# Kernel tuning notes

Hardware: AMD Instinct MI355X
Metric: run time of the kernel (lower is better)

The kernel has to match this reference:

```python
import jax, jax.numpy as jnp
import numpy as np

V, F, P = 1024, 2048, 8192
_EPS = 1e-12


def setup_inputs() -> dict:
    key = jax.random.key(0)
    kv, kf, kp = jax.random.split(key, 3)
    verts = jax.random.normal(kv, (V, 3), dtype=jnp.float32)
    faces = jax.random.randint(kf, (F, 3), 0, V, dtype=jnp.int32)
    points = jax.random.normal(kp, (P, 3), dtype=jnp.float32)
    return {"verts": verts, "faces": faces, "points": points}


def _closest_point_on_tri(p, a, b, c):
    """Ericson's closest-point-on-triangle, broadcast over leading dims.
    p, a, b, c: [..., 3] -> closest point [..., 3]."""
    ab = b - a
    ac = c - a
    ap = p - a
    d1 = jnp.sum(ab * ap, -1)
    d2 = jnp.sum(ac * ap, -1)
    bp = p - b
    d3 = jnp.sum(ab * bp, -1)
    d4 = jnp.sum(ac * bp, -1)
    cp = p - c
    d5 = jnp.sum(ab * cp, -1)
    d6 = jnp.sum(ac * cp, -1)
    vc = d1 * d4 - d3 * d2
    vb = d5 * d2 - d1 * d6
    va = d3 * d6 - d5 * d4
    # guarded edge/interior parameters (denominators are >0 whenever the
    # corresponding region condition holds; eps keeps unselected branches finite)
    t_ab = d1 / jnp.maximum(d1 - d3, _EPS)
    t_ac = d2 / jnp.maximum(d2 - d6, _EPS)
    t_bc = (d4 - d3) / jnp.maximum((d4 - d3) + (d5 - d6), _EPS)
    denom = jnp.maximum(va + vb + vc, _EPS)
    v_in = vb / denom
    w_in = vc / denom
    # first-match region selection (vertex A, vertex B, edge AB, vertex C, edge AC, edge BC, interior)
    cA = (d1 <= 0) & (d2 <= 0)
    cB = (d3 >= 0) & (d4 <= d3)
    cAB = (vc <= 0) & (d1 >= 0) & (d3 <= 0)
    cC = (d6 >= 0) & (d5 <= d6)
    cAC = (vb <= 0) & (d2 >= 0) & (d6 <= 0)
    cBC = (va <= 0) & ((d4 - d3) >= 0) & ((d5 - d6) >= 0)
    z = jnp.zeros_like(d1)
    o = jnp.ones_like(d1)
    bv = jnp.select([cA, cB, cAB, cC, cAC, cBC], [z, o, t_ab, z, z, 1.0 - t_bc], v_in)
    bw = jnp.select([cA, cB, cAB, cC, cAC, cBC], [z, z, z, o, t_ac, t_bc], w_in)
    bu = 1.0 - bv - bw
    return a * bu[..., None] + b * bv[..., None] + c * bw[..., None]


def reference(verts, faces, points):
    tri = verts[faces]  # [F, 3, 3]
    a = tri[:, 0][None]  # [1, F, 3]
    b = tri[:, 1][None]
    c = tri[:, 2][None]
    cp = _closest_point_on_tri(points[:, None, :], a, b, c)  # [P, F, 3]
    dist2 = jnp.sum((points[:, None, :] - cp) ** 2, -1)  # [P, F] squared distances
    assoc = jnp.argmin(dist2, axis=1).astype(jnp.int32)  # [P] nearest triangle index
    dist = jnp.min(dist2, axis=1)  # [P]
    # loss_type == 'mse': kernel loss = sum(dist), then *= 1000 / P
    loss = jnp.sum(dist) * (1000.0 / points.shape[0])
    return loss, dist, assoc
```

## Files before the change

kernel.cpp:

```cpp
#include <hip/hip_runtime.h>
#include <float.h>

#define P_TOTAL 8192
#define F_TOTAL 2048
#define TPB     256
#define CHUNK   256
#define HALF_T  (F_TOTAL / 2)
#define NCHUNK  (HALF_T / CHUNK)

__device__ __forceinline__ float refine_rcp(float D) {
#pragma clang fp contract(off)
    float r0 = __builtin_amdgcn_rcpf(D);
    float e1 = __builtin_fmaf(-D, r0, 1.0f);
    return __builtin_fmaf(e1, r0, r0);
}
__device__ __forceinline__ float div_rn(float num, float D, float r) {
#pragma clang fp contract(off)
    float q0 = num * r;
    float e  = __builtin_fmaf(-D, q0, num);
    return __builtin_fmaf(e, r, q0);
}

__device__ __forceinline__ void region_select(
    float d1, float d2, float d3, float d4, float d5, float d6,
    float va, float vb, float vc, float d43, float d56,
    float g1, float g2, float g3, float g4,
    float& bu, float& bv, float& bw)
{
#pragma clang fp contract(off)
    float G1 = fmaxf(g1, 1e-12f);
    float G2 = fmaxf(g2, 1e-12f);
    float G3 = fmaxf(g3, 1e-12f);
    float G4 = fmaxf(g4, 1e-12f);

    bool cA  = (d1 <= 0.f) & (d2 <= 0.f);
    bool cB  = (d3 >= 0.f) & (d4 <= d3);
    bool cAB = (vc <= 0.f) & (d1 >= 0.f) & (d3 <= 0.f);
    bool cC  = (d6 >= 0.f) & (d5 <= d6);
    bool cAC = (vb <= 0.f) & (d2 >= 0.f) & (d6 <= 0.f);
    bool cBC = (va <= 0.f) & (d43 >= 0.f) & (d56 >= 0.f);

    float nv = cA ? 0.f : cB ? 1.f : cAB ? d1 : cC ? 0.f
             : cAC ? 0.f : cBC ? d43 : vb;
    float nw = cA ? 0.f : cB ? 0.f : cAB ? 0.f : cC ? 1.f
             : cAC ? d2 : cBC ? d43 : vc;
    float D  = cA ? 1.f : cB ? 1.f : cAB ? G1 : cC ? 1.f
             : cAC ? G2 : cBC ? G3 : G4;
    bool fBC = cBC && !(cA || cB || cAB || cC || cAC);

    float r   = refine_rcp(D);
    float qv  = div_rn(nv, D, r);
    float bww = div_rn(nw, D, r);
    float bvv = fBC ? (1.0f - qv) : qv;
    bv = bvv; bw = bww;
    bu = (1.0f - bvv) - bww;
}

__device__ __forceinline__ float eval_exact(
    float px, float py, float pz, float4 q0, float4 q1, float4 q2)
{
#pragma clang fp contract(off)
    float ax = q0.x, ay = q0.y, az = q0.z;
    float bx = q0.w, by = q1.x, bz = q1.y;
    float cx = q1.z, cy = q1.w, cz = q2.x;

    float abx = bx - ax, aby = by - ay, abz = bz - az;
    float acx = cx - ax, acy = cy - ay, acz = cz - az;
    float apx = px - ax, apy = py - ay, apz = pz - az;
    float d1 = (abx * apx + aby * apy) + abz * apz;
    float d2 = (acx * apx + acy * apy) + acz * apz;
    float bpx = px - bx, bpy = py - by, bpz = pz - bz;
    float d3 = (abx * bpx + aby * bpy) + abz * bpz;
    float d4 = (acx * bpx + acy * bpy) + acz * bpz;
    float cpx = px - cx, cpy = py - cy, cpz = pz - cz;
    float d5 = (abx * cpx + aby * cpy) + abz * cpz;
    float d6 = (acx * cpx + acy * cpy) + acz * cpz;

    float vc = d1 * d4 - d3 * d2;
    float vb = d5 * d2 - d1 * d6;
    float va = d3 * d6 - d5 * d4;
    float d43 = d4 - d3, d56 = d5 - d6;
    float g1 = d1 - d3, g2 = d2 - d6, g3 = d43 + d56, g4 = (va + vb) + vc;

    float bu, bv, bw;
    region_select(d1, d2, d3, d4, d5, d6, va, vb, vc, d43, d56,
                  g1, g2, g3, g4, bu, bv, bw);

    float cpx2 = (ax * bu + bx * bv) + cx * bw;
    float cpy2 = (ay * bu + by * bv) + cy * bw;
    float cpz2 = (az * bu + bz * bv) + cz * bw;
    float dx = px - cpx2, dy = py - cpy2, dz = pz - cpz2;
    return (dx * dx + dy * dy) + dz * dz;
}

__global__ __launch_bounds__(256) void msdf_prep(
    const float* __restrict__ verts, const int* __restrict__ faces,
    float4* __restrict__ pre_n, float4* __restrict__ pre_v,
    float4* __restrict__ pre_a)
{
    int t = blockIdx.x * 256 + threadIdx.x;
    int i0 = faces[3 * t + 0], i1 = faces[3 * t + 1], i2 = faces[3 * t + 2];
    float ax = verts[3 * i0], ay = verts[3 * i0 + 1], az = verts[3 * i0 + 2];
    float bx = verts[3 * i1], by = verts[3 * i1 + 1], bz = verts[3 * i1 + 2];
    float cx = verts[3 * i2], cy = verts[3 * i2 + 1], cz = verts[3 * i2 + 2];
    float e1x = bx - ax, e1y = by - ay, e1z = bz - az;
    float e2x = cx - ax, e2y = cy - ay, e2z = cz - az;
    float nx = e1y * e2z - e1z * e2y;
    float ny = e1z * e2x - e1x * e2z;
    float nz = e1x * e2y - e1y * e2x;
    float nn = (nx * nx + ny * ny) + nz * nz;
    float inv = (nn > 1e-30f) ? (1.0f / sqrtf(nn)) : 0.0f;
    nx *= inv; ny *= inv; nz *= inv;
    pre_n[t] = make_float4(nx, ny, nz, (nx * ax + ny * ay) + nz * az);
    pre_v[3 * t + 0] = make_float4(ax, ay, az, bx);
    pre_v[3 * t + 1] = make_float4(by, bz, cx, cy);
    pre_v[3 * t + 2] = make_float4(cz, 0.f, 0.f, 0.f);
    pre_a[t] = make_float4(ax, ay, az, 0.f);
}

#define FLUSH_BODY(take) do {                                             \
    int j = (lane < (take)) ? lane : 0;                                   \
    int t = slist[w][(h + j) & 511];                                      \
    float4 q0 = pre_v[3 * t + 0];                                         \
    float4 q1 = pre_v[3 * t + 1];                                         \
    float4 q2 = pre_v[3 * t + 2];                                         \
    float d2v = eval_exact(px, py, pz, q0, q1, q2);                       \
    unsigned int bits = __float_as_uint(d2v);                             \
    if (bits < best_bits) { best_bits = bits; best_idx = t; }             \
    ubloc = fminf(ubloc, d2v);                                            \
    h += (take); pend -= (take);                                          \
} while (0)

__global__ __launch_bounds__(TPB) void msdf_main(
    const float4* __restrict__ pre_n, const float4* __restrict__ pre_v,
    const float4* __restrict__ pre_a,
    const float* __restrict__ points, float* __restrict__ out)
{
    __shared__ int slist[4][512];
    __shared__ unsigned long long keys[4];
    const int tid  = threadIdx.x;
    const int lane = tid & 63;
    const int w    = tid >> 6;
    const int p    = blockIdx.x * 2 + (w >> 1);
    const int tb   = (w & 1) * HALF_T;

    const float px = points[3 * p], py = points[3 * p + 1], pz = points[3 * p + 2];

    float u = FLT_MAX;
    #pragma unroll
    for (int s = 0; s < 4; ++s) {
        float4 q = pre_a[tb + s * 64 + lane];
        float dx = px - q.x, dy = py - q.y, dz = pz - q.z;
        u = fminf(u, (dx * dx + dy * dy) + dz * dz);
    }
    #pragma unroll
    for (int off = 32; off; off >>= 1)
        u = fminf(u, __shfl_xor(u, off, 64));
    float ub = u;

    unsigned int best_bits = 0xFFFFFFFFu;
    int best_idx = 0;
    int pend = 0, h = 0;

    for (int c = 0; c < NCHUNK; ++c) {
        const float ubm = ub * 1.02f + 1e-18f;
        #pragma unroll
        for (int s = 0; s < 4; ++s) {
            int t = tb + c * CHUNK + s * 64 + lane;
            float4 n = pre_n[t];
            float lv = ((n.x * px + n.y * py) + n.z * pz) - n.w;
            bool pred = (lv * lv <= ubm);
            unsigned long long m = __ballot(pred);
            if (pred) {
                int off = (int)__popcll(m & ((1ull << lane) - 1ull));
                slist[w][(h + pend + off) & 511] = t;
            }
            pend += (int)__popcll(m);
        }

        bool drain = (c == 0) || (c == NCHUNK - 1);
        if (pend >= 64 || (drain && pend > 0)) {
            float ubloc = FLT_MAX;
            while (pend >= 64) FLUSH_BODY(64);
            if (drain && pend > 0) FLUSH_BODY(pend);
            #pragma unroll
            for (int off = 32; off; off >>= 1)
                ubloc = fminf(ubloc, __shfl_xor(ubloc, off, 64));
            ub = fminf(ub, ubloc);
        }
    }

    unsigned long long key =
        ((unsigned long long)best_bits << 32) | (unsigned int)best_idx;
    #pragma unroll
    for (int off = 32; off > 0; off >>= 1) {
        unsigned int hi = (unsigned int)(key >> 32);
        unsigned int lo = (unsigned int)(key & 0xFFFFFFFFu);
        unsigned int ohi = __shfl_down(hi, off, 64);
        unsigned int olo = __shfl_down(lo, off, 64);
        unsigned long long ok = ((unsigned long long)ohi << 32) | olo;
        key = (ok < key) ? ok : key;
    }
    if (lane == 0) keys[w] = key;
    __syncthreads();
    if (tid < 2) {
        unsigned long long k0 = keys[2 * tid];
        unsigned long long k1 = keys[2 * tid + 1];
        unsigned long long km = (k1 < k0) ? k1 : k0;
        int pp = blockIdx.x * 2 + tid;
        out[1 + pp]           = __uint_as_float((unsigned int)(km >> 32));
        out[1 + P_TOTAL + pp] = (float)(unsigned int)(km & 0xFFFFFFFFu);
    }
}

__global__ __launch_bounds__(256) void msdf_loss(float* __restrict__ out)
{
    __shared__ float wsum[4];
    float s = 0.f;
    for (int k = 0; k < P_TOTAL / 256; ++k)
        s += out[1 + k * 256 + threadIdx.x];
    #pragma unroll
    for (int off = 32; off > 0; off >>= 1) s += __shfl_down(s, off, 64);
    int lane = threadIdx.x & 63, w = threadIdx.x >> 6;
    if (lane == 0) wsum[w] = s;
    __syncthreads();
    if (threadIdx.x == 0) {
        float tot = ((wsum[0] + wsum[1]) + wsum[2]) + wsum[3];
        out[0] = tot * (1000.0f / (float)P_TOTAL);
    }
}

extern "C" void kernel_launch(void* const* d_in, const int* in_sizes, int n_in,
                              void* d_out, int out_size, void* d_ws, size_t ws_size,
                              hipStream_t stream) {
    const float* verts  = (const float*)d_in[0];
    const int*   faces  = (const int*)d_in[1];
    const float* points = (const float*)d_in[2];
    float* out = (float*)d_out;
    float4* pre_n = (float4*)d_ws;
    float4* pre_v = (float4*)((char*)d_ws + F_TOTAL * 16);
    float4* pre_a = (float4*)((char*)d_ws + F_TOTAL * 16 * 4);

    msdf_prep<<<dim3(F_TOTAL / 256), dim3(256), 0, stream>>>(verts, faces, pre_n, pre_v, pre_a);
    msdf_main<<<dim3(P_TOTAL / 2), dim3(TPB), 0, stream>>>(pre_n, pre_v, pre_a, points, out);
    msdf_loss<<<dim3(1), dim3(256), 0, stream>>>(out);
}
```

Before: 87.18 us.

## Split each point across four waves and fuse loss via last-block reduction

```diff
diff --git a/kernel.cpp b/kernel.cpp
--- a/kernel.cpp
+++ b/kernel.cpp
@@ -5,8 +5,10 @@
 #define F_TOTAL 2048
 #define TPB     256
 #define CHUNK   256
-#define HALF_T  (F_TOTAL / 2)
-#define NCHUNK  (HALF_T / CHUNK)
+#define QUART_T (F_TOTAL / 4)
+#define NCHUNK  (QUART_T / CHUNK)
+
+__device__ unsigned int g_cnt;
 
 __device__ __forceinline__ float refine_rcp(float D) {
 #pragma clang fp contract(off)
@@ -98,6 +100,7 @@
     float4* __restrict__ pre_n, float4* __restrict__ pre_v,
     float4* __restrict__ pre_a)
 {
+    if (blockIdx.x == 0 && threadIdx.x == 0) g_cnt = 0u;
     int t = blockIdx.x * 256 + threadIdx.x;
     int i0 = faces[3 * t + 0], i1 = faces[3 * t + 1], i2 = faces[3 * t + 2];
     float ax = verts[3 * i0], ay = verts[3 * i0 + 1], az = verts[3 * i0 + 2];
@@ -138,11 +141,14 @@
 {
     __shared__ int slist[4][512];
     __shared__ unsigned long long keys[4];
+    __shared__ float ubsh[4];
+    __shared__ float wsum[4];
+    __shared__ int amLast;
     const int tid  = threadIdx.x;
     const int lane = tid & 63;
     const int w    = tid >> 6;
-    const int p    = blockIdx.x * 2 + (w >> 1);
-    const int tb   = (w & 1) * HALF_T;
+    const int p    = blockIdx.x;
+    const int tb   = w * QUART_T;
 
     const float px = points[3 * p], py = points[3 * p + 1], pz = points[3 * p + 2];
 
@@ -156,7 +162,9 @@
     #pragma unroll
     for (int off = 32; off; off >>= 1)
         u = fminf(u, __shfl_xor(u, off, 64));
-    float ub = u;
+    if (lane == 0) ubsh[w] = u;
+    __syncthreads();
+    float ub = fminf(fminf(ubsh[0], ubsh[1]), fminf(ubsh[2], ubsh[3]));
 
     unsigned int best_bits = 0xFFFFFFFFu;
     int best_idx = 0;
@@ -178,15 +186,18 @@
             pend += (int)__popcll(m);
         }
 
-        bool drain = (c == 0) || (c == NCHUNK - 1);
-        if (pend >= 64 || (drain && pend > 0)) {
-            float ubloc = FLT_MAX;
-            while (pend >= 64) FLUSH_BODY(64);
-            if (drain && pend > 0) FLUSH_BODY(pend);
-            #pragma unroll
-            for (int off = 32; off; off >>= 1)
-                ubloc = fminf(ubloc, __shfl_xor(ubloc, off, 64));
-            ub = fminf(ub, ubloc);
+        float ubloc = FLT_MAX;
+        while (pend >= 64) FLUSH_BODY(64);
+        if (pend > 0) FLUSH_BODY(pend);
+        #pragma unroll
+        for (int off = 32; off; off >>= 1)
+            ubloc = fminf(ubloc, __shfl_xor(ubloc, off, 64));
+        ub = fminf(ub, ubloc);
+
+        if (c == 0) {
+            if (lane == 0) ubsh[w] = ub;
+            __syncthreads();
+            ub = fminf(fminf(ubsh[0], ubsh[1]), fminf(ubsh[2], ubsh[3]));
         }
     }
 
@@ -203,30 +214,32 @@
     }
     if (lane == 0) keys[w] = key;
     __syncthreads();
-    if (tid < 2) {
-        unsigned long long k0 = keys[2 * tid];
-        unsigned long long k1 = keys[2 * tid + 1];
-        unsigned long long km = (k1 < k0) ? k1 : k0;
-        int pp = blockIdx.x * 2 + tid;
-        out[1 + pp]           = __uint_as_float((unsigned int)(km >> 32));
-        out[1 + P_TOTAL + pp] = (float)(unsigned int)(km & 0xFFFFFFFFu);
-    }
-}
-
-__global__ __launch_bounds__(256) void msdf_loss(float* __restrict__ out)
-{
-    __shared__ float wsum[4];
-    float s = 0.f;
-    for (int k = 0; k < P_TOTAL / 256; ++k)
-        s += out[1 + k * 256 + threadIdx.x];
-    #pragma unroll
-    for (int off = 32; off > 0; off >>= 1) s += __shfl_down(s, off, 64);
-    int lane = threadIdx.x & 63, w = threadIdx.x >> 6;
-    if (lane == 0) wsum[w] = s;
+    if (tid == 0) {
+        unsigned long long k0 = keys[0], k1 = keys[1];
+        unsigned long long k2 = keys[2], k3 = keys[3];
+        unsigned long long ka = (k1 < k0) ? k1 : k0;
+        unsigned long long kb = (k3 < k2) ? k3 : k2;
+        unsigned long long km = (kb < ka) ? kb : ka;
+        out[1 + p]           = __uint_as_float((unsigned int)(km >> 32));
+        out[1 + P_TOTAL + p] = (float)(unsigned int)(km & 0xFFFFFFFFu);
+        __threadfence();
+        amLast = (atomicAdd(&g_cnt, 1u) == (unsigned int)(gridDim.x - 1));
+    }
     __syncthreads();
-    if (threadIdx.x == 0) {
-        float tot = ((wsum[0] + wsum[1]) + wsum[2]) + wsum[3];
-        out[0] = tot * (1000.0f / (float)P_TOTAL);
+
+    if (amLast) {
+        __threadfence();
+        float s = 0.f;
+        for (int k = 0; k < P_TOTAL / 256; ++k)
+            s += out[1 + k * 256 + tid];
+        #pragma unroll
+        for (int off = 32; off > 0; off >>= 1) s += __shfl_down(s, off, 64);
+        if (lane == 0) wsum[w] = s;
+        __syncthreads();
+        if (tid == 0) {
+            float tot = ((wsum[0] + wsum[1]) + wsum[2]) + wsum[3];
+            out[0] = tot * (1000.0f / (float)P_TOTAL);
+        }
     }
 }
 
@@ -242,6 +255,5 @@
     float4* pre_a = (float4*)((char*)d_ws + F_TOTAL * 16 * 4);
 
     msdf_prep<<<dim3(F_TOTAL / 256), dim3(256), 0, stream>>>(verts, faces, pre_n, pre_v, pre_a);
-    msdf_main<<<dim3(P_TOTAL / 2), dim3(TPB), 0, stream>>>(pre_n, pre_v, pre_a, points, out);
-    msdf_loss<<<dim3(1), dim3(256), 0, stream>>>(out);
-}
+    msdf_main<<<dim3(P_TOTAL), dim3(TPB), 0, stream>>>(pre_n, pre_v, pre_a, points, out);
+}
```

After: 234.3 us. +168.8%, slower.

## Spatially sort triangles into cells and cull 64-triangle groups by bounding spheres

Applied to the files above, without the earlier changes.

```diff
diff --git a/kernel.cpp b/kernel.cpp
--- a/kernel.cpp
+++ b/kernel.cpp
@@ -4,9 +4,10 @@
 #define P_TOTAL 8192
 #define F_TOTAL 2048
 #define TPB     256
-#define CHUNK   256
-#define HALF_T  (F_TOTAL / 2)
-#define NCHUNK  (HALF_T / CHUNK)
+#define NGROUP  32
+#define GPW     16
+#define NCHUNK  4
+#define NCELL   64
 
 __device__ __forceinline__ float refine_rcp(float D) {
 #pragma clang fp contract(off)
@@ -93,29 +94,101 @@
     return (dx * dx + dy * dy) + dz * dz;
 }
 
-__global__ __launch_bounds__(256) void msdf_prep(
+__global__ __launch_bounds__(1024) void msdf_prep(
     const float* __restrict__ verts, const int* __restrict__ faces,
     float4* __restrict__ pre_n, float4* __restrict__ pre_v,
-    float4* __restrict__ pre_a)
-{
-    int t = blockIdx.x * 256 + threadIdx.x;
-    int i0 = faces[3 * t + 0], i1 = faces[3 * t + 1], i2 = faces[3 * t + 2];
-    float ax = verts[3 * i0], ay = verts[3 * i0 + 1], az = verts[3 * i0 + 2];
-    float bx = verts[3 * i1], by = verts[3 * i1 + 1], bz = verts[3 * i1 + 2];
-    float cx = verts[3 * i2], cy = verts[3 * i2 + 1], cz = verts[3 * i2 + 2];
-    float e1x = bx - ax, e1y = by - ay, e1z = bz - az;
-    float e2x = cx - ax, e2y = cy - ay, e2z = cz - az;
-    float nx = e1y * e2z - e1z * e2y;
-    float ny = e1z * e2x - e1x * e2z;
-    float nz = e1x * e2y - e1y * e2x;
-    float nn = (nx * nx + ny * ny) + nz * nz;
-    float inv = (nn > 1e-30f) ? (1.0f / sqrtf(nn)) : 0.0f;
-    nx *= inv; ny *= inv; nz *= inv;
-    pre_n[t] = make_float4(nx, ny, nz, (nx * ax + ny * ay) + nz * az);
-    pre_v[3 * t + 0] = make_float4(ax, ay, az, bx);
-    pre_v[3 * t + 1] = make_float4(by, bz, cx, cy);
-    pre_v[3 * t + 2] = make_float4(cz, 0.f, 0.f, 0.f);
-    pre_a[t] = make_float4(ax, ay, az, 0.f);
+    float4* __restrict__ pre_a, float4* __restrict__ spheres)
+{
+    __shared__ int s_cur[NCELL];
+    __shared__ int s_base[NCELL];
+    const int tid = threadIdx.x;
+    if (tid < NCELL) s_cur[tid] = 0;
+    __syncthreads();
+
+    float vtx[2][9];
+    float4 pl[2];
+    int   cl[2];
+    #pragma unroll
+    for (int i = 0; i < 2; ++i) {
+        int t = tid + i * 1024;
+        int i0 = faces[3 * t + 0], i1 = faces[3 * t + 1], i2 = faces[3 * t + 2];
+        float ax = verts[3 * i0], ay = verts[3 * i0 + 1], az = verts[3 * i0 + 2];
+        float bx = verts[3 * i1], by = verts[3 * i1 + 1], bz = verts[3 * i1 + 2];
+        float cx = verts[3 * i2], cy = verts[3 * i2 + 1], cz = verts[3 * i2 + 2];
+        float e1x = bx - ax, e1y = by - ay, e1z = bz - az;
+        float e2x = cx - ax, e2y = cy - ay, e2z = cz - az;
+        float nx = e1y * e2z - e1z * e2y;
+        float ny = e1z * e2x - e1x * e2z;
+        float nz = e1x * e2y - e1y * e2x;
+        float nn = (nx * nx + ny * ny) + nz * nz;
+        float inv = (nn > 1e-30f) ? (1.0f / sqrtf(nn)) : 0.0f;
+        nx *= inv; ny *= inv; nz *= inv;
+        pl[i] = make_float4(nx, ny, nz, (nx * ax + ny * ay) + nz * az);
+        vtx[i][0] = ax; vtx[i][1] = ay; vtx[i][2] = az;
+        vtx[i][3] = bx; vtx[i][4] = by; vtx[i][5] = bz;
+        vtx[i][6] = cx; vtx[i][7] = cy; vtx[i][8] = cz;
+        float cxm = (ax + bx + cx) * (1.0f / 3.0f);
+        float cym = (ay + by + cy) * (1.0f / 3.0f);
+        float czm = (az + bz + cz) * (1.0f / 3.0f);
+        int ix = min(max((int)floorf((cxm + 3.0f) * (4.0f / 6.0f)), 0), 3);
+        int iy = min(max((int)floorf((cym + 3.0f) * (4.0f / 6.0f)), 0), 3);
+        int iz = min(max((int)floorf((czm + 3.0f) * (4.0f / 6.0f)), 0), 3);
+        cl[i] = (ix & 1) | ((iy & 1) << 1) | ((iz & 1) << 2)
+              | ((ix >> 1) << 3) | ((iy >> 1) << 4) | ((iz >> 1) << 5);
+        atomicAdd(&s_cur[cl[i]], 1);
+    }
+    __syncthreads();
+    if (tid == 0) {
+        int a = 0;
+        for (int i = 0; i < NCELL; ++i) { int c = s_cur[i]; s_base[i] = a; a += c; }
+    }
+    __syncthreads();
+    if (tid < NCELL) s_cur[tid] = s_base[tid];
+    __syncthreads();
+    #pragma unroll
+    for (int i = 0; i < 2; ++i) {
+        int t = tid + i * 1024;
+        int pos = atomicAdd(&s_cur[cl[i]], 1);
+        pre_n[pos] = pl[i];
+        pre_v[3 * pos + 0] = make_float4(vtx[i][0], vtx[i][1], vtx[i][2], vtx[i][3]);
+        pre_v[3 * pos + 1] = make_float4(vtx[i][4], vtx[i][5], vtx[i][6], vtx[i][7]);
+        pre_v[3 * pos + 2] = make_float4(vtx[i][8], __int_as_float(t), 0.f, 0.f);
+        pre_a[pos] = make_float4(vtx[i][0], vtx[i][1], vtx[i][2], 0.f);
+    }
+    __threadfence();
+    __syncthreads();
+
+    const int wv = tid >> 6, lane = tid & 63;
+    for (int g = wv; g < NGROUP; g += 16) {
+        int t = g * 64 + lane;
+        float4 q0 = pre_v[3 * t + 0];
+        float4 q1 = pre_v[3 * t + 1];
+        float4 q2 = pre_v[3 * t + 2];
+        float ax2 = q0.x, ay2 = q0.y, az2 = q0.z;
+        float bx2 = q0.w, by2 = q1.x, bz2 = q1.y;
+        float cx2 = q1.z, cy2 = q1.w, cz2 = q2.x;
+        float sx = (ax2 + bx2 + cx2) * (1.0f / 3.0f);
+        float sy = (ay2 + by2 + cy2) * (1.0f / 3.0f);
+        float sz = (az2 + bz2 + cz2) * (1.0f / 3.0f);
+        #pragma unroll
+        for (int off = 32; off; off >>= 1) {
+            sx += __shfl_xor(sx, off, 64);
+            sy += __shfl_xor(sy, off, 64);
+            sz += __shfl_xor(sz, off, 64);
+        }
+        float ccx = sx * (1.0f / 64.0f), ccy = sy * (1.0f / 64.0f), ccz = sz * (1.0f / 64.0f);
+        float dax = ax2 - ccx, day = ay2 - ccy, daz = az2 - ccz;
+        float dbx = bx2 - ccx, dby = by2 - ccy, dbz = bz2 - ccz;
+        float dcx = cx2 - ccx, dcy = cy2 - ccy, dcz = cz2 - ccz;
+        float r2 = fmaxf(fmaxf((dax*dax+day*day)+daz*daz,
+                               (dbx*dbx+dby*dby)+dbz*dbz),
+                               (dcx*dcx+dcy*dcy)+dcz*dcz);
+        #pragma unroll
+        for (int off = 32; off; off >>= 1)
+            r2 = fmaxf(r2, __shfl_xor(r2, off, 64));
+        if (lane == 0)
+            spheres[g] = make_float4(ccx, ccy, ccz, sqrtf(r2) * 1.0001f + 1e-6f);
+    }
 }
 
 #define FLUSH_BODY(take) do {                                             \
@@ -125,15 +198,18 @@
     float4 q1 = pre_v[3 * t + 1];                                         \
     float4 q2 = pre_v[3 * t + 2];                                         \
     float d2v = eval_exact(px, py, pz, q0, q1, q2);                       \
+    int oi = __float_as_int(q2.y);                                        \
     unsigned int bits = __float_as_uint(d2v);                             \
-    if (bits < best_bits) { best_bits = bits; best_idx = t; }             \
+    if (bits < best_bits || (bits == best_bits && oi < best_idx)) {       \
+        best_bits = bits; best_idx = oi;                                  \
+    }                                                                     \
     ubloc = fminf(ubloc, d2v);                                            \
     h += (take); pend -= (take);                                          \
 } while (0)
 
 __global__ __launch_bounds__(TPB) void msdf_main(
     const float4* __restrict__ pre_n, const float4* __restrict__ pre_v,
-    const float4* __restrict__ pre_a,
+    const float4* __restrict__ pre_a, const float4* __restrict__ spheres,
     const float* __restrict__ points, float* __restrict__ out)
 {
     __shared__ int slist[4][512];
@@ -142,14 +218,23 @@
     const int lane = tid & 63;
     const int w    = tid >> 6;
     const int p    = blockIdx.x * 2 + (w >> 1);
-    const int tb   = (w & 1) * HALF_T;
+    const int par  = w & 1;
 
     const float px = points[3 * p], py = points[3 * p + 1], pz = points[3 * p + 2];
 
+    float lb2;
+    {
+        float4 s = spheres[2 * (lane & 15) + par];
+        float dx = px - s.x, dy = py - s.y, dz = pz - s.z;
+        float dc = sqrtf((dx * dx + dy * dy) + dz * dz);
+        float lb = fmaxf(dc - s.w, 0.f);
+        lb2 = lb * lb;
+    }
+
     float u = FLT_MAX;
     #pragma unroll
     for (int s = 0; s < 4; ++s) {
-        float4 q = pre_a[tb + s * 64 + lane];
+        float4 q = pre_a[8 * (s * 64 + lane)];
         float dx = px - q.x, dy = py - q.y, dz = pz - q.z;
         u = fminf(u, (dx * dx + dy * dy) + dz * dz);
     }
@@ -159,23 +244,27 @@
     float ub = u;
 
     unsigned int best_bits = 0xFFFFFFFFu;
-    int best_idx = 0;
+    int best_idx = 0x7FFFFFFF;
     int pend = 0, h = 0;
 
     for (int c = 0; c < NCHUNK; ++c) {
         const float ubm = ub * 1.02f + 1e-18f;
+        unsigned long long bm = __ballot((lane < GPW) && (lb2 <= ubm));
         #pragma unroll
-        for (int s = 0; s < 4; ++s) {
-            int t = tb + c * CHUNK + s * 64 + lane;
-            float4 n = pre_n[t];
-            float lv = ((n.x * px + n.y * py) + n.z * pz) - n.w;
-            bool pred = (lv * lv <= ubm);
-            unsigned long long m = __ballot(pred);
-            if (pred) {
-                int off = (int)__popcll(m & ((1ull << lane) - 1ull));
-                slist[w][(h + pend + off) & 511] = t;
+        for (int k = 0; k < 4; ++k) {
+            if ((bm >> (4 * c + k)) & 1ull) {
+                int g = 2 * (4 * c + k) + par;
+                int t = g * 64 + lane;
+                float4 n = pre_n[t];
+                float lv = ((n.x * px + n.y * py) + n.z * pz) - n.w;
+                bool pred = (lv * lv <= ubm);
+                unsigned long long m = __ballot(pred);
+                if (pred) {
+                    int off = (int)__popcll(m & ((1ull << lane) - 1ull));
+                    slist[w][(h + pend + off) & 511] = t;
+                }
+                pend += (int)__popcll(m);
             }
-            pend += (int)__popcll(m);
         }
 
         bool drain = (c == 0) || (c == NCHUNK - 1);
@@ -237,11 +326,12 @@
     const int*   faces  = (const int*)d_in[1];
     const float* points = (const float*)d_in[2];
     float* out = (float*)d_out;
-    float4* pre_n = (float4*)d_ws;
-    float4* pre_v = (float4*)((char*)d_ws + F_TOTAL * 16);
-    float4* pre_a = (float4*)((char*)d_ws + F_TOTAL * 16 * 4);
-
-    msdf_prep<<<dim3(F_TOTAL / 256), dim3(256), 0, stream>>>(verts, faces, pre_n, pre_v, pre_a);
-    msdf_main<<<dim3(P_TOTAL / 2), dim3(TPB), 0, stream>>>(pre_n, pre_v, pre_a, points, out);
+    float4* pre_n   = (float4*)d_ws;
+    float4* pre_v   = (float4*)((char*)d_ws + F_TOTAL * 16);
+    float4* pre_a   = (float4*)((char*)d_ws + F_TOTAL * 16 * 4);
+    float4* spheres = (float4*)((char*)d_ws + F_TOTAL * 16 * 5);
+
+    msdf_prep<<<dim3(1), dim3(1024), 0, stream>>>(verts, faces, pre_n, pre_v, pre_a, spheres);
+    msdf_main<<<dim3(P_TOTAL / 2), dim3(TPB), 0, stream>>>(pre_n, pre_v, pre_a, spheres, points, out);
     msdf_loss<<<dim3(1), dim3(256), 0, stream>>>(out);
 }
```

Result: slower. 106.5 us (+22.1%).

## Process two query points per wavefront to reuse triangle plane loads

Applied to the files above, without the earlier changes.

```diff
diff --git a/kernel.cpp b/kernel.cpp
--- a/kernel.cpp
+++ b/kernel.cpp
@@ -118,17 +118,17 @@
     pre_a[t] = make_float4(ax, ay, az, 0.f);
 }
 
-#define FLUSH_BODY(take) do {                                             \
+#define FLUSH_BODY(SL, PX, PY, PZ, BB, BI, H, PEND, UBL, take) do {       \
     int j = (lane < (take)) ? lane : 0;                                   \
-    int t = slist[w][(h + j) & 511];                                      \
+    int t = slist[SL][((H) + j) & 511];                                   \
     float4 q0 = pre_v[3 * t + 0];                                         \
     float4 q1 = pre_v[3 * t + 1];                                         \
     float4 q2 = pre_v[3 * t + 2];                                         \
-    float d2v = eval_exact(px, py, pz, q0, q1, q2);                       \
+    float d2v = eval_exact(PX, PY, PZ, q0, q1, q2);                       \
     unsigned int bits = __float_as_uint(d2v);                             \
-    if (bits < best_bits) { best_bits = bits; best_idx = t; }             \
-    ubloc = fminf(ubloc, d2v);                                            \
-    h += (take); pend -= (take);                                          \
+    if (bits < (BB)) { (BB) = bits; (BI) = t; }                           \
+    (UBL) = fminf((UBL), d2v);                                            \
+    (H) += (take); (PEND) -= (take);                                      \
 } while (0)
 
 __global__ __launch_bounds__(TPB) void msdf_main(
@@ -136,78 +136,116 @@
     const float4* __restrict__ pre_a,
     const float* __restrict__ points, float* __restrict__ out)
 {
-    __shared__ int slist[4][512];
-    __shared__ unsigned long long keys[4];
+    __shared__ int slist[8][512];
+    __shared__ unsigned long long keys[8];
     const int tid  = threadIdx.x;
     const int lane = tid & 63;
     const int w    = tid >> 6;
-    const int p    = blockIdx.x * 2 + (w >> 1);
-    const int tb   = (w & 1) * HALF_T;
-
-    const float px = points[3 * p], py = points[3 * p + 1], pz = points[3 * p + 2];
-
-    float u = FLT_MAX;
+    const int pair = w >> 1;
+    const int half = w & 1;
+    const int pa   = blockIdx.x * 4 + 2 * pair;
+    const int tb   = half * HALF_T;
+
+    const float pax = points[3 * pa + 0], pay = points[3 * pa + 1], paz = points[3 * pa + 2];
+    const float pbx = points[3 * pa + 3], pby = points[3 * pa + 4], pbz = points[3 * pa + 5];
+
+    float uA = FLT_MAX, uB = FLT_MAX;
     #pragma unroll
     for (int s = 0; s < 4; ++s) {
         float4 q = pre_a[tb + s * 64 + lane];
-        float dx = px - q.x, dy = py - q.y, dz = pz - q.z;
-        u = fminf(u, (dx * dx + dy * dy) + dz * dz);
-    }
-    #pragma unroll
-    for (int off = 32; off; off >>= 1)
-        u = fminf(u, __shfl_xor(u, off, 64));
-    float ub = u;
-
-    unsigned int best_bits = 0xFFFFFFFFu;
-    int best_idx = 0;
-    int pend = 0, h = 0;
+        float dax = pax - q.x, day = pay - q.y, daz = paz - q.z;
+        uA = fminf(uA, (dax * dax + day * day) + daz * daz);
+        float dbx = pbx - q.x, dby = pby - q.y, dbz = pbz - q.z;
+        uB = fminf(uB, (dbx * dbx + dby * dby) + dbz * dbz);
+    }
+    #pragma unroll
+    for (int off = 32; off; off >>= 1) {
+        uA = fminf(uA, __shfl_xor(uA, off, 64));
+        uB = fminf(uB, __shfl_xor(uB, off, 64));
+    }
+    float ubA = uA, ubB = uB;
+
+    unsigned int bbA = 0xFFFFFFFFu, bbB = 0xFFFFFFFFu;
+    int biA = 0, biB = 0;
+    int pendA = 0, hA = 0, pendB = 0, hB = 0;
 
     for (int c = 0; c < NCHUNK; ++c) {
-        const float ubm = ub * 1.02f + 1e-18f;
+        const float ubmA = ubA * 1.02f + 1e-18f;
+        const float ubmB = ubB * 1.02f + 1e-18f;
         #pragma unroll
         for (int s = 0; s < 4; ++s) {
             int t = tb + c * CHUNK + s * 64 + lane;
             float4 n = pre_n[t];
-            float lv = ((n.x * px + n.y * py) + n.z * pz) - n.w;
-            bool pred = (lv * lv <= ubm);
-            unsigned long long m = __ballot(pred);
-            if (pred) {
-                int off = (int)__popcll(m & ((1ull << lane) - 1ull));
-                slist[w][(h + pend + off) & 511] = t;
+            float lvA = ((n.x * pax + n.y * pay) + n.z * paz) - n.w;
+            float lvB = ((n.x * pbx + n.y * pby) + n.z * pbz) - n.w;
+            bool prA = (lvA * lvA <= ubmA);
+            bool prB = (lvB * lvB <= ubmB);
+            unsigned long long mA = __ballot(prA);
+            unsigned long long mB = __ballot(prB);
+            if (prA) {
+                int off = (int)__popcll(mA & ((1ull << lane) - 1ull));
+                slist[2 * w + 0][(hA + pendA + off) & 511] = t;
             }
-            pend += (int)__popcll(m);
+            pendA += (int)__popcll(mA);
+            if (prB) {
+                int off = (int)__popcll(mB & ((1ull << lane) - 1ull));
+                slist[2 * w + 1][(hB + pendB + off) & 511] = t;
+            }
+            pendB += (int)__popcll(mB);
         }
 
         bool drain = (c == 0) || (c == NCHUNK - 1);
-        if (pend >= 64 || (drain && pend > 0)) {
+        if (pendA >= 64 || (drain && pendA > 0)) {
             float ubloc = FLT_MAX;
-            while (pend >= 64) FLUSH_BODY(64);
-            if (drain && pend > 0) FLUSH_BODY(pend);
+            while (pendA >= 64)
+                FLUSH_BODY(2 * w + 0, pax, pay, paz, bbA, biA, hA, pendA, ubloc, 64);
+            if (drain && pendA > 0)
+                FLUSH_BODY(2 * w + 0, pax, pay, paz, bbA, biA, hA, pendA, ubloc, pendA);
             #pragma unroll
             for (int off = 32; off; off >>= 1)
                 ubloc = fminf(ubloc, __shfl_xor(ubloc, off, 64));
-            ub = fminf(ub, ubloc);
+            ubA = fminf(ubA, ubloc);
         }
-    }
-
-    unsigned long long key =
-        ((unsigned long long)best_bits << 32) | (unsigned int)best_idx;
+        if (pendB >= 64 || (drain && pendB > 0)) {
+            float ubloc = FLT_MAX;
+            while (pendB >= 64)
+                FLUSH_BODY(2 * w + 1, pbx, pby, pbz, bbB, biB, hB, pendB, ubloc, 64);
+            if (drain && pendB > 0)
+                FLUSH_BODY(2 * w + 1, pbx, pby, pbz, bbB, biB, hB, pendB, ubloc, pendB);
+            #pragma unroll
+            for (int off = 32; off; off >>= 1)
+                ubloc = fminf(ubloc, __shfl_xor(ubloc, off, 64));
+            ubB = fminf(ubB, ubloc);
+        }
+    }
+
+    unsigned long long keyA =
+        ((unsigned long long)bbA << 32) | (unsigned int)biA;
+    unsigned long long keyB =
+        ((unsigned long long)bbB << 32) | (unsigned int)biB;
     #pragma unroll
     for (int off = 32; off > 0; off >>= 1) {
-        unsigned int hi = (unsigned int)(key >> 32);
-        unsigned int lo = (unsigned int)(key & 0xFFFFFFFFu);
-        unsigned int ohi = __shfl_down(hi, off, 64);
-        unsigned int olo = __shfl_down(lo, off, 64);
-        unsigned long long ok = ((unsigned long long)ohi << 32) | olo;
-        key = (ok < key) ? ok : key;
-    }
-    if (lane == 0) keys[w] = key;
+        unsigned int hiA = (unsigned int)(keyA >> 32);
+        unsigned int loA = (unsigned int)(keyA & 0xFFFFFFFFu);
+        unsigned int ohiA = __shfl_down(hiA, off, 64);
+        unsigned int oloA = __shfl_down(loA, off, 64);
+        unsigned long long okA = ((unsigned long long)ohiA << 32) | oloA;
+        keyA = (okA < keyA) ? okA : keyA;
+        unsigned int hiB = (unsigned int)(keyB >> 32);
+        unsigned int loB = (unsigned int)(keyB & 0xFFFFFFFFu);
+        unsigned int ohiB = __shfl_down(hiB, off, 64);
+        unsigned int oloB = __shfl_down(loB, off, 64);
+        unsigned long long okB = ((unsigned long long)ohiB << 32) | oloB;
+        keyB = (okB < keyB) ? okB : keyB;
+    }
+    if (lane == 0) { keys[2 * w + 0] = keyA; keys[2 * w + 1] = keyB; }
     __syncthreads();
-    if (tid < 2) {
-        unsigned long long k0 = keys[2 * tid];
-        unsigned long long k1 = keys[2 * tid + 1];
+    if (tid < 4) {
+        int pr = tid >> 1, j = tid & 1;
+        unsigned long long k0 = keys[2 * (2 * pr + 0) + j];
+        unsigned long long k1 = keys[2 * (2 * pr + 1) + j];
         unsigned long long km = (k1 < k0) ? k1 : k0;
-        int pp = blockIdx.x * 2 + tid;
+        int pp = blockIdx.x * 4 + 2 * pr + j;
         out[1 + pp]           = __uint_as_float((unsigned int)(km >> 32));
         out[1 + P_TOTAL + pp] = (float)(unsigned int)(km & 0xFFFFFFFFu);
     }
@@ -242,6 +280,6 @@
     float4* pre_a = (float4*)((char*)d_ws + F_TOTAL * 16 * 4);
 
     msdf_prep<<<dim3(F_TOTAL / 256), dim3(256), 0, stream>>>(verts, faces, pre_n, pre_v, pre_a);
-    msdf_main<<<dim3(P_TOTAL / 2), dim3(TPB), 0, stream>>>(pre_n, pre_v, pre_a, points, out);
+    msdf_main<<<dim3(P_TOTAL / 4), dim3(TPB), 0, stream>>>(pre_n, pre_v, pre_a, points, out);
     msdf_loss<<<dim3(1), dim3(256), 0, stream>>>(out);
 }
```

New measurement: 89.71 us. 2.9% more time.
